# Kernel optimization log

Hardware: AMD Instinct MI355X
Metric: run time of the kernel (lower is better)

The kernel has to match this reference:

```python
import jax, jax.numpy as jnp
from jax import lax
import numpy as np

DIM, K, OUT_DIM = 128, 64, 256
SAMPLE_STEP = 30  # eval mode
WIN = 200


def _l2n(v, axis):
    return v / jnp.maximum(jnp.linalg.norm(v, axis=axis, keepdims=True), 1e-12)


def _conv(x, w, b, pad):
    y = lax.conv_general_dilated(x, w, (1, 1), [(pad, pad), (pad, pad)],
                                 dimension_numbers=('NCHW', 'OIHW', 'NCHW'))
    return y + b[None, :, None, None]


def _maxpool(x, kh, kw, sh, sw, ph, pw):
    return lax.reduce_window(x, -jnp.inf, lax.max, (1, 1, kh, kw), (1, 1, sh, sw),
                             [(0, 0), (0, 0), (ph, ph), (pw, pw)])


def setup_inputs() -> dict:
    key = jax.random.key(0)
    ks = jax.random.split(key, 12)
    s = 1.0 / np.sqrt(DIM)
    return {
        'x': jax.random.normal(ks[0], (4, DIM, 48, 900), jnp.float32),
        'cluster_centers': jax.random.uniform(ks[1], (K, DIM), jnp.float32) * s,
        'conv_w': jax.random.normal(ks[2], (K, DIM), jnp.float32) * s * 0.1,
        'conv_b': jax.random.normal(ks[3], (K,), jnp.float32) * s * 0.1,
        'w1': jax.random.normal(ks[4], (2 * DIM, DIM, 5, 5), jnp.float32) * 0.02,
        'b1': jnp.zeros((2 * DIM,), jnp.float32),
        'w2': jax.random.normal(ks[5], (4 * DIM, 2 * DIM, 5, 5), jnp.float32) * 0.01,
        'b2': jnp.zeros((4 * DIM,), jnp.float32),
        'w3': jax.random.normal(ks[6], (8 * DIM, 4 * DIM, 5, 5), jnp.float32) * 0.01,
        'b3': jnp.zeros((8 * DIM,), jnp.float32),
        'mlp_w': jax.random.normal(ks[7], (OUT_DIM, DIM * (K + 8)), jnp.float32) * s * 0.01,
        'mlp_b': jax.random.normal(ks[8], (OUT_DIM,), jnp.float32) * s * 0.01,
    }


def reference(x, cluster_centers, conv_w, conv_b, w1, b1, w2, b2, w3, b3, mlp_w, mlp_b):
    N, C, H, W = x.shape  # (4, 128, 48, 900)
    # ---- soft assignment (1x1 conv), softmax over clusters ----
    logits = jnp.einsum('nchw,kc->nkhw', x, conv_w) + conv_b[None, :, None, None]
    a = jax.nn.softmax(logits, axis=1)  # softmax over K (per spatial pos)
    # ---- residual-weighted sum over H, fused (avoids (N,K,C,HW) tensor) ----
    # sum_h a[n,k,h,w] * (x[n,c,h,w] - centers[k,c])
    xa = jnp.einsum('nkhw,nchw->nkcw', a, x)
    a_sum = a.sum(axis=2)  # (N,K,W)
    res = xa - cluster_centers[None, :, :, None] * a_sum[:, :, None, :]  # (N,K,C,W)
    # ---- x_conv feature branch on circularly padded input ----
    xp = jnp.concatenate([x[..., 800:], x, x[..., :100]], axis=-1)  # (N,C,H,1100)
    h = jax.nn.leaky_relu(_conv(xp, w1, b1, 2), 0.2)
    h = _maxpool(h, 3, 3, 3, 1, 0, 1)          # (N,256,16,1100)
    h = jax.nn.leaky_relu(_conv(h, w2, b2, 2), 0.2)
    h = _maxpool(h, 4, 5, 4, 1, 0, 2)          # (N,512,4,1100)
    h = _conv(h, w3, b3, 2)
    h = _maxpool(h, 4, WIN, 4, 1, 0, 0)        # (N,1024,1,901)
    xf = h[:, :, 0, ::SAMPLE_STEP][..., :-1]   # (N,1024,30)
    xf = _l2n(jnp.transpose(xf, (0, 2, 1)), axis=2)  # (N,30,1024)
    n_win = xf.shape[1]
    # ---- windowed VLAD pooling via cumsum (equiv to unfold(200, step).sum) ----
    resp = jnp.concatenate([res[..., 800:], res, res[..., :100]], axis=-1)  # (N,K,C,1100)
    cs = jnp.concatenate([jnp.zeros_like(resp[..., :1]), jnp.cumsum(resp, axis=-1)], axis=-1)
    starts = jnp.arange(n_win) * SAMPLE_STEP  # last window dropped, matching [:-1]
    vlad = cs[..., starts + WIN] - cs[..., starts]  # (N,K,C,30)
    vlad = jnp.transpose(vlad, (0, 3, 1, 2))        # (N,30,K,C)
    vlad = _l2n(vlad, axis=3)                        # intra-norm per cluster
    vlad = _l2n(vlad.reshape(N * n_win, K * C), axis=1)
    feat = jnp.concatenate([vlad, xf.reshape(N * n_win, -1)], axis=1)  # (N*30, 9216)
    out = _l2n(feat @ mlp_w.T + mlp_b, axis=1)
    return out.reshape(N, n_win, -1)
```

## Files before the change

### kernel.cpp

```cpp
#include <hip/hip_runtime.h>
#include <hip/hip_bf16.h>

#define NB   4
#define DIM  128
#define KC   64
#define HH   48
#define WW   900
#define WPAD 1100
#define WST  1160
#define NT   30
#define OC1  256
#define OC2  512
#define OC3  1024

typedef __attribute__((ext_vector_type(8))) short bf16x8;
typedef __attribute__((ext_vector_type(4))) float f32x4;
typedef unsigned short u16;
typedef unsigned int u32;

__device__ __forceinline__ u16 f2bf(float f){
  __hip_bfloat16 h = __float2bfloat16(f);
  u16 u; __builtin_memcpy(&u, &h, 2); return u;
}
__device__ __forceinline__ float bf2f(u16 u){
  __hip_bfloat16 h; __builtin_memcpy(&h, &u, 2); return __bfloat162float(h);
}

typedef __attribute__((address_space(1))) const u32 g_u32;
typedef __attribute__((address_space(3))) u32 l_u32;
__device__ __forceinline__ void gll16(const void* g, void* l){
  __builtin_amdgcn_global_load_lds((g_u32*)g, (l_u32*)l, 16, 0, 0);
}


__global__ __launch_bounds__(256) void vlad_softmax(const float* __restrict__ x,
    const float* __restrict__ conv_w, const float* __restrict__ conv_b, float* __restrict__ a){
  __shared__ float cwT[DIM*KC];
  __shared__ float cbs[KC];
  int t = threadIdx.x;
  for (int i = t; i < DIM*KC; i += 256){ int c = i >> 6, k = i & 63; cwT[i] = conv_w[k*DIM + c]; }
  if (t < KC) cbs[t] = conv_b[t];
  __syncthreads();
  int w = blockIdx.x*256 + t, h = blockIdx.y, n = blockIdx.z;
  bool ok = (w < WW);
  float lg[KC];
  #pragma unroll
  for (int k = 0; k < KC; ++k) lg[k] = cbs[k];
  const float* xp = x + (size_t)n*DIM*HH*WW + (size_t)h*WW + (ok ? w : 0);
  for (int c = 0; c < DIM; ++c){
    float xv = ok ? xp[(size_t)c*HH*WW] : 0.f;
    const float* cw = &cwT[c*KC];
    #pragma unroll
    for (int k = 0; k < KC; ++k) lg[k] += xv * cw[k];
  }
  float m = lg[0];
  #pragma unroll
  for (int k = 1; k < KC; ++k) m = fmaxf(m, lg[k]);
  float s = 0.f;
  #pragma unroll
  for (int k = 0; k < KC; ++k){ lg[k] = __expf(lg[k]-m); s += lg[k]; }
  float inv = 1.f/s;
  if (ok){
    float* dst = a + (((size_t)(n*HH + h))*WW + w)*KC;
    #pragma unroll
    for (int k = 0; k < KC; k += 4){
      float4 v = make_float4(lg[k]*inv, lg[k+1]*inv, lg[k+2]*inv, lg[k+3]*inv);
      *(float4*)&dst[k] = v;
    }
  }
}

__global__ __launch_bounds__(256) void vlad_xa3(const float* __restrict__ x, const float* __restrict__ a,
    const float* __restrict__ centers, float* __restrict__ ps){
  __shared__ float xw[2][10][132];
  __shared__ float aw[2][10][64];
  int t = threadIdx.x, s = blockIdx.x, n = blockIdx.y;
  int k = t >> 2, cb4 = t & 3;
  int p0 = s*10;
  int w0 = (p0 < 100) ? p0 + 800 : ((p0 < 1000) ? p0 - 100 : p0 - 1000);
  const float* xn = x + (size_t)n*DIM*HH*WW + w0;
  const float* an = a + (size_t)n*HH*WW*KC + (size_t)w0*KC;

  auto load = [&](int h, int buf){
    if (t < 128){
      const float* xr = xn + ((size_t)t*HH + h)*WW;
      #pragma unroll
      for (int w = 0; w < 10; ++w) xw[buf][w][t] = xr[w];
    } else {
      const float* ar = an + (size_t)h*WW*KC;
      int e0 = (t - 128)*5;
      #pragma unroll
      for (int q = 0; q < 5; ++q){ int e = e0 + q; aw[buf][e >> 6][e & 63] = ar[e]; }
    }
  };

  float acc[32];
  #pragma unroll
  for (int j = 0; j < 32; ++j) acc[j] = 0.f;
  float Sacc = 0.f;

  load(0, 0);
  for (int h = 0; h < HH; ++h){
    int buf = h & 1;
    __syncthreads();
    if (h + 1 < HH) load(h + 1, buf ^ 1);
    #pragma unroll 2
    for (int w = 0; w < 10; ++w){
      float av = aw[buf][w][k];
      Sacc += av;
      const float4* xr4 = (const float4*)&xw[buf][w][cb4*32];
      #pragma unroll
      for (int jj = 0; jj < 8; ++jj){
        float4 xv = xr4[jj];
        acc[jj*4+0] += av*xv.x; acc[jj*4+1] += av*xv.y;
        acc[jj*4+2] += av*xv.z; acc[jj*4+3] += av*xv.w;
      }
    }
    __syncthreads();
  }

  const float* ck = centers + (size_t)k*DIM + cb4*32;
  float* dst = ps + (((size_t)(n*KC + k))*110 + s)*DIM + cb4*32;
  #pragma unroll
  for (int jj = 0; jj < 8; ++jj){
    float4 o;
    o.x = acc[jj*4+0] - ck[jj*4+0]*Sacc;
    o.y = acc[jj*4+1] - ck[jj*4+1]*Sacc;
    o.z = acc[jj*4+2] - ck[jj*4+2]*Sacc;
    o.w = acc[jj*4+3] - ck[jj*4+3]*Sacc;
    *(float4*)&dst[jj*4] = o;
  }
}

__global__ __launch_bounds__(128) void vlad_win2(const float* __restrict__ ps, float* __restrict__ vlad){
  int c = threadIdx.x, k = blockIdx.x, tt = blockIdx.y, n = blockIdx.z;
  const float* base = ps + ((size_t)(n*KC + k))*110*DIM + c;
  float v = 0.f;
  #pragma unroll
  for (int u = 0; u < 20; ++u) v += base[(3*tt + u)*DIM];
  float ss = v*v;
  #pragma unroll
  for (int m = 1; m < 64; m <<= 1) ss += __shfl_xor(ss, m);
  __shared__ float red[2];
  if ((c & 63) == 0) red[c >> 6] = ss;
  __syncthreads();
  float tot = red[0] + red[1];
  float inv = 1.f / fmaxf(sqrtf(tot), 1e-12f);
  vlad[(((size_t)(n*NT + tt))*KC + k)*DIM + c] = v*inv;
}

__global__ __launch_bounds__(256) void vlad_gnorm(float* __restrict__ vlad){
  int row = blockIdx.x, t = threadIdx.x;
  float4* v = (float4*)(vlad + (size_t)row*(KC*DIM));
  float4 r[8]; float ss = 0.f;
  #pragma unroll
  for (int i = 0; i < 8; ++i){
    r[i] = v[t + i*256];
    ss += r[i].x*r[i].x + r[i].y*r[i].y + r[i].z*r[i].z + r[i].w*r[i].w;
  }
  #pragma unroll
  for (int m = 1; m < 64; m <<= 1) ss += __shfl_xor(ss, m);
  __shared__ float red[4];
  if ((t & 63) == 0) red[t >> 6] = ss;
  __syncthreads();
  float tot = red[0]+red[1]+red[2]+red[3];
  float inv = 1.f / fmaxf(sqrtf(tot), 1e-12f);
  #pragma unroll
  for (int i = 0; i < 8; ++i){
    float4 o = r[i]; o.x*=inv; o.y*=inv; o.z*=inv; o.w*=inv;
    v[t + i*256] = o;
  }
}


__global__ __launch_bounds__(256) void build_xpb(const float* __restrict__ x, u16* __restrict__ xpb){
  __shared__ u16 tile[DIM][33];
  int t = threadIdx.x, h = blockIdx.y, n = blockIdx.z;
  int b0 = blockIdx.x*32;
  #pragma unroll
  for (int i = 0; i < 16; ++i){
    int e = t + i*256;
    int c = e >> 5, bl = e & 31;
    int b = b0 + bl, w = b - 2;
    float v = 0.f;
    if (w >= 0 && w < WPAD){
      int wsrc = (w + 800) % 900;
      v = x[((size_t)(n*DIM + c)*HH + h)*WW + wsrc];
    }
    tile[c][bl] = f2bf(v);
  }
  __syncthreads();
  #pragma unroll
  for (int i = 0; i < 16; ++i){
    int e = t + i*256;
    int bl = e >> 7, c = e & 127;
    int b = b0 + bl;
    if (b < WST) xpb[((size_t)(n*HH + h)*WST + b)*DIM + c] = tile[c][bl];
  }
}

__global__ __launch_bounds__(256) void pack_w2(const float* __restrict__ w, u16* __restrict__ wp,
    int OC, int IC, int NICB){
  int idx = blockIdx.x*256 + threadIdx.x;
  int total = OC*IC*25;
  if (idx >= total) return;
  int e = idx & 7;
  int q = idx >> 3;
  int oc = q % OC;  int q2 = q / OC;
  int lgp = q2 & 3; int k0i = (q2 >> 2) & 3;
  int q3 = q2 >> 4;
  int icb = q3 % NICB; int tap = q3 / NICB;
  int ic = icb*128 + k0i*32 + lgp*8 + e;
  wp[idx] = f2bf(w[((size_t)oc*IC + ic)*25 + tap]);
}

template<int IC, int OC, int H>
__global__ __launch_bounds__(256,2) void conv5x5(const u16* __restrict__ in, const u16* __restrict__ wp,
    const float* __restrict__ bias, u16* __restrict__ out){
  constexpr int NICB = IC/128;
  constexpr int LN = (NICB==1?0:(NICB==2?1:2));
  __shared__ u16 sIn[2][132*128];
  int t = threadIdx.x;
  int wave = t >> 6, lane = t & 63, lr = lane & 15, lgp = lane >> 4;
  int w0  = blockIdx.x * 128;
  int ocb = blockIdx.y * 256;
  int nh = blockIdx.z; int n = nh / H, h = nh % H;
  int wo_oc = wave*64;
  f32x4 acc[4][8] = {};
  const u16* inN = in + (size_t)n*H*WST*IC;
  const size_t laneA = (size_t)(ocb + wo_oc + lr)*8;
  int dhlo = (2-h > 0) ? (2-h) : 0;
  int dhhi = (H+1-h < 4) ? (H+1-h) : 4;
  int nslab = (dhhi - dhlo + 1) << LN;

  auto stage = [&](int slab_, int buf_){
    int dh = dhlo + (slab_ >> LN);
    int icb = slab_ & (NICB-1);
    const u16* rowbase = inN + (size_t)(h + dh - 2)*WST*IC + (size_t)icb*128;
    for (int i = wave; i < 33; i += 4){
      int qq = i*64 + lane;
      int r = qq >> 4, cp = qq & 15;
      int c = cp ^ (r & 7);
      gll16(rowbase + (size_t)(w0 + r)*IC + c*8, &sIn[buf_][i*512]);
    }
  };

  stage(0, 0);
  __syncthreads();

  for (int slab = 0; slab < nslab; ++slab){
    int buf = slab & 1;
    if (slab + 1 < nslab) stage(slab + 1, buf ^ 1);
    int dh = dhlo + (slab >> LN);
    int icb = slab & (NICB-1);
    const u16* wslab = wp + (size_t)(dh*5*NICB + icb)*16*OC*8 + laneA;
    const u16* sB = &sIn[buf][0];
    bf16x8 Abuf[3][4];
    #pragma unroll
    for (int pi = 0; pi < 2; ++pi){
      const u16* ap = wslab + (size_t)((pi >> 2)*NICB*16 + ((pi & 3)*4 + lgp))*OC*8;
      #pragma unroll
      for (int ja = 0; ja < 4; ++ja) Abuf[pi][ja] = *(const bf16x8*)(ap + (size_t)ja*16*8);
    }
    #pragma unroll
    for (int dw = 0; dw < 5; ++dw){
      #pragma unroll
      for (int k0i = 0; k0i < 4; ++k0i){
        constexpr int NI = 20;
        const int i = dw*4 + k0i;
        {
          const int pn = (i + 2 < NI) ? (i + 2) : (NI - 1);
          const u16* ap = wslab + (size_t)((pn >> 2)*NICB*16 + ((pn & 3)*4 + lgp))*OC*8;
          #pragma unroll
          for (int ja = 0; ja < 4; ++ja) Abuf[(i + 2) % 3][ja] = *(const bf16x8*)(ap + (size_t)ja*16*8);
        }
        bf16x8 B[8];
        #pragma unroll
        for (int jb = 0; jb < 8; ++jb){
          int br = jb*16 + lr + dw;
          B[jb] = *(const bf16x8*)&sB[br*128 + (((k0i*4 + lgp) ^ (br & 7)) << 3)];
        }
        __builtin_amdgcn_s_setprio(1);
        #pragma unroll
        for (int ja = 0; ja < 4; ++ja)
          #pragma unroll
          for (int jb = 0; jb < 8; ++jb)
            acc[ja][jb] = __builtin_amdgcn_mfma_f32_16x16x32_bf16(Abuf[i % 3][ja], B[jb], acc[ja][jb], 0, 0, 0);
        __builtin_amdgcn_s_setprio(0);
      }
    }
    __syncthreads();
  }

  u16* outP = out + ((size_t)(n*H + h)*WST + 2)*OC;
  #pragma unroll
  for (int ja = 0; ja < 4; ++ja){
    int oc = ocb + wo_oc + ja*16 + lgp*4;
    float4 bv = *(const float4*)&bias[oc];
    #pragma unroll
    for (int jb = 0; jb < 8; ++jb){
      int wg = w0 + jb*16 + lr;
      if (wg < WPAD){
        f32x4 av = acc[ja][jb];
        ushort4 o;
        o.x = f2bf(av[0] + bv.x);
        o.y = f2bf(av[1] + bv.y);
        o.z = f2bf(av[2] + bv.z);
        o.w = f2bf(av[3] + bv.w);
        *(ushort4*)(outP + (size_t)wg*OC + oc) = o;
      }
    }
  }
}

__global__ __launch_bounds__(256) void pool1k(const u16* __restrict__ in, u16* __restrict__ out){
  int t = threadIdx.x;
  int wb = blockIdx.x*4 + (t >> 6);
  int oc = (t & 63)*4;
  int ho = blockIdx.y, n = blockIdx.z;
  int wo = wb - 2;
  float m0=0.f,m1=0.f,m2=0.f,m3=0.f;
  if (wo >= 0 && wo < WPAD){
    m0=m1=m2=m3=-1e30f;
    #pragma unroll
    for (int kh = 0; kh < 3; ++kh){
      const u16* row = in + ((size_t)(n*HH + ho*3 + kh)*WST + 2)*OC1 + oc;
      #pragma unroll
      for (int kw = 0; kw < 3; ++kw){
        int wi = wo - 1 + kw;
        if (wi >= 0 && wi < WPAD){
          ushort4 v = *(const ushort4*)(row + (size_t)wi*OC1);
          m0 = fmaxf(m0, bf2f(v.x)); m1 = fmaxf(m1, bf2f(v.y));
          m2 = fmaxf(m2, bf2f(v.z)); m3 = fmaxf(m3, bf2f(v.w));
        }
      }
    }
    m0 = (m0>0.f)?m0:0.2f*m0; m1 = (m1>0.f)?m1:0.2f*m1;
    m2 = (m2>0.f)?m2:0.2f*m2; m3 = (m3>0.f)?m3:0.2f*m3;
  }
  ushort4 o; o.x=f2bf(m0); o.y=f2bf(m1); o.z=f2bf(m2); o.w=f2bf(m3);
  *(ushort4*)(out + ((size_t)(n*16 + ho)*WST + wb)*OC1 + oc) = o;
}

__global__ __launch_bounds__(256) void pool2k(const u16* __restrict__ in, u16* __restrict__ out){
  int t = threadIdx.x;
  int wb = blockIdx.x*2 + (t >> 7);
  int oc = (t & 127)*4;
  int ho = blockIdx.y, n = blockIdx.z;
  int wo = wb - 2;
  float m0=0.f,m1=0.f,m2=0.f,m3=0.f;
  if (wo >= 0 && wo < WPAD){
    m0=m1=m2=m3=-1e30f;
    #pragma unroll
    for (int kh = 0; kh < 4; ++kh){
      const u16* row = in + ((size_t)(n*16 + ho*4 + kh)*WST + 2)*OC2 + oc;
      #pragma unroll
      for (int kw = 0; kw < 5; ++kw){
        int wi = wo - 2 + kw;
        if (wi >= 0 && wi < WPAD){
          ushort4 v = *(const ushort4*)(row + (size_t)wi*OC2);
          m0 = fmaxf(m0, bf2f(v.x)); m1 = fmaxf(m1, bf2f(v.y));
          m2 = fmaxf(m2, bf2f(v.z)); m3 = fmaxf(m3, bf2f(v.w));
        }
      }
    }
    m0 = (m0>0.f)?m0:0.2f*m0; m1 = (m1>0.f)?m1:0.2f*m1;
    m2 = (m2>0.f)?m2:0.2f*m2; m3 = (m3>0.f)?m3:0.2f*m3;
  }
  ushort4 o; o.x=f2bf(m0); o.y=f2bf(m1); o.z=f2bf(m2); o.w=f2bf(m3);
  *(ushort4*)(out + ((size_t)(n*4 + ho)*WST + wb)*OC2 + oc) = o;
}

__global__ __launch_bounds__(256) void pool3k(const u16* __restrict__ in, float* __restrict__ xfraw){
  int tt = blockIdx.x, hh = blockIdx.y, n = blockIdx.z;
  int oc = threadIdx.x*4;
  float m0=-1e30f,m1=-1e30f,m2=-1e30f,m3=-1e30f;
  const u16* row = in + ((size_t)(n*4 + hh)*WST + 2 + 30*tt)*OC3 + oc;
  for (int p = 0; p < 200; ++p){
    ushort4 v = *(const ushort4*)(row + (size_t)p*OC3);
    m0 = fmaxf(m0, bf2f(v.x)); m1 = fmaxf(m1, bf2f(v.y));
    m2 = fmaxf(m2, bf2f(v.z)); m3 = fmaxf(m3, bf2f(v.w));
  }
  float* dst = xfraw + (((size_t)(n*NT + tt))*4 + hh)*OC3 + oc;
  dst[0]=m0; dst[1]=m1; dst[2]=m2; dst[3]=m3;
}

__global__ __launch_bounds__(256) void xf_norm(const float* __restrict__ xfraw, float* __restrict__ xf){
  int row = blockIdx.x, t = threadIdx.x;
  const float* src = xfraw + (size_t)row*4096;
  float v[4]; float ss = 0.f;
  #pragma unroll
  for (int j = 0; j < 4; ++j){
    float m = src[t + j*256];
    #pragma unroll
    for (int hh = 1; hh < 4; ++hh) m = fmaxf(m, src[hh*1024 + t + j*256]);
    v[j] = m; ss += m*m;
  }
  #pragma unroll
  for (int m = 1; m < 64; m <<= 1) ss += __shfl_xor(ss, m);
  __shared__ float red[4];
  if ((t & 63) == 0) red[t >> 6] = ss;
  __syncthreads();
  float tot = red[0]+red[1]+red[2]+red[3];
  float inv = 1.f/fmaxf(sqrtf(tot), 1e-12f);
  float* dst = xf + (size_t)row*OC3;
  #pragma unroll
  for (int j = 0; j < 4; ++j) dst[t + j*256] = v[j]*inv;
}

__global__ __launch_bounds__(256) void mlp_part(const float* __restrict__ vlad, const float* __restrict__ xf,
    const float* __restrict__ W, float* __restrict__ part){
  __shared__ float feat[4][256];
  int kc = blockIdx.x, rb = blockIdx.y, t = threadIdx.x;
  int i0 = kc*256;
  #pragma unroll
  for (int r = 0; r < 4; ++r){
    int row = rb*4 + r;
    int i = i0 + t;
    feat[r][t] = (i < 8192) ? vlad[(size_t)row*8192 + i] : xf[(size_t)row*1024 + (i - 8192)];
  }
  __syncthreads();
  const float* wr = W + (size_t)t*9216 + i0;
  float a0=0.f, a1=0.f, a2=0.f, a3=0.f;
  for (int i = 0; i < 256; i += 4){
    float4 wv = *(const float4*)&wr[i];
    a0 += feat[0][i]*wv.x + feat[0][i+1]*wv.y + feat[0][i+2]*wv.z + feat[0][i+3]*wv.w;
    a1 += feat[1][i]*wv.x + feat[1][i+1]*wv.y + feat[1][i+2]*wv.z + feat[1][i+3]*wv.w;
    a2 += feat[2][i]*wv.x + feat[2][i+1]*wv.y + feat[2][i+2]*wv.z + feat[2][i+3]*wv.w;
    a3 += feat[3][i]*wv.x + feat[3][i+1]*wv.y + feat[3][i+2]*wv.z + feat[3][i+3]*wv.w;
  }
  float* p0 = part + (((size_t)(rb*4 + 0)*36 + kc))*256 + t;
  p0[0]          = a0;
  p0[36*256]     = a1;
  p0[2*36*256]   = a2;
  p0[3*36*256]   = a3;
}

__global__ __launch_bounds__(256) void mlp_reduce(const float* __restrict__ part, const float* __restrict__ b,
    float* __restrict__ out){
  int row = blockIdx.x, t = threadIdx.x;
  const float* pr = part + (size_t)row*36*256 + t;
  float acc = b[t];
  #pragma unroll
  for (int kc = 0; kc < 36; ++kc) acc += pr[kc*256];
  float ss = acc*acc;
  #pragma unroll
  for (int m = 1; m < 64; m <<= 1) ss += __shfl_xor(ss, m);
  __shared__ float red[4];
  if ((t & 63) == 0) red[t >> 6] = ss;
  __syncthreads();
  float tot = red[0]+red[1]+red[2]+red[3];
  float inv = 1.f/fmaxf(sqrtf(tot), 1e-12f);
  out[(size_t)row*256 + t] = acc*inv;
}

extern "C" void kernel_launch(void* const* d_in, const int* in_sizes, int n_in,
                              void* d_out, int out_size, void* d_ws, size_t ws_size,
                              hipStream_t stream){
  const float* x       = (const float*)d_in[0];
  const float* centers = (const float*)d_in[1];
  const float* conv_w  = (const float*)d_in[2];
  const float* conv_b  = (const float*)d_in[3];
  const float* w1      = (const float*)d_in[4];
  const float* b1      = (const float*)d_in[5];
  const float* w2      = (const float*)d_in[6];
  const float* b2      = (const float*)d_in[7];
  const float* w3      = (const float*)d_in[8];
  const float* b3      = (const float*)d_in[9];
  const float* mlp_w   = (const float*)d_in[10];
  const float* mlp_b   = (const float*)d_in[11];
  float* out = (float*)d_out;
  char* ws = (char*)d_ws;
  const size_t MB = 1ull << 20;
  if (ws_size < 248*MB) return;

  float* vlad  = (float*)(ws + 0);
  float* xf    = (float*)(ws + 4*MB);
  float* xfraw = (float*)(ws + 5*MB);
  char*  AR    = ws + 7*MB;
  float* a  = (float*)(AR + 85*MB);
  float* ps = (float*)(AR + 128*MB);
  u16* xpb = (u16*)(AR + 0);
  u16* wp1 = (u16*)(AR + 55*MB);
  u16* wp2 = (u16*)(AR + 57*MB);
  u16* wp3 = (u16*)(AR + 64*MB);
  u16* h1  = (u16*)(AR + 89*MB);
  u16* p1  = (u16*)(AR + 0);
  u16* h2  = (u16*)(AR + 89*MB);
  u16* p2  = (u16*)(AR + 163*MB);
  u16* h3  = (u16*)(AR + 0);
  float* part = (float*)(AR + 200*MB);

  vlad_softmax<<<dim3(4,HH,NB), 256, 0, stream>>>(x, conv_w, conv_b, a);
  vlad_xa3<<<dim3(110,NB), 256, 0, stream>>>(x, a, centers, ps);
  vlad_win2<<<dim3(KC,NT,NB), 128, 0, stream>>>(ps, vlad);
  vlad_gnorm<<<dim3(NB*NT), 256, 0, stream>>>(vlad);

  pack_w2<<<dim3(3200),  256, 0, stream>>>(w1, wp1, OC1, DIM, 1);
  pack_w2<<<dim3(12800), 256, 0, stream>>>(w2, wp2, OC2, OC1, 2);
  pack_w2<<<dim3(51200), 256, 0, stream>>>(w3, wp3, OC3, OC2, 4);
  build_xpb<<<dim3(37,HH,NB), 256, 0, stream>>>(x, xpb);
  conv5x5<128,256,48><<<dim3(9, OC1/256, NB*HH), 256, 0, stream>>>(xpb, wp1, b1, h1);
  pool1k<<<dim3(WST/4,16,NB), 256, 0, stream>>>(h1, p1);
  conv5x5<256,512,16><<<dim3(9, OC2/256, NB*16), 256, 0, stream>>>(p1, wp2, b2, h2);
  pool2k<<<dim3(WST/2,4,NB), 256, 0, stream>>>(h2, p2);
  conv5x5<512,1024,4><<<dim3(9, OC3/256, NB*4), 256, 0, stream>>>(p2, wp3, b3, h3);
  pool3k<<<dim3(NT,4,NB), 256, 0, stream>>>(h3, xfraw);
  xf_norm<<<dim3(NB*NT), 256, 0, stream>>>(xfraw, xf);

  mlp_part<<<dim3(36,30), 256, 0, stream>>>(vlad, xf, mlp_w, part);
  mlp_reduce<<<dim3(NB*NT), 256, 0, stream>>>(part, mlp_b, out);
}
```

Baseline: 1.574 ms.

## Remap conv blocks per XCD, deepen weight prefetch, split final pool into segments

The conv kernel now uses a flattened 1D grid. Blocks are remapped so that blocks on the same XCD (bid&7) share the same output-channel tile, which should improve L2 reuse of the packed weights. The weight register prefetch ring grows from depth 3 to 5 and now carries across slab boundaries, hiding global-load latency between slabs at the cost of more VGPRs. The final 200-wide max-pool is restructured into 10-column segment maxima reduced over H, then combined 20 at a time in xf_norm, which avoids re-reading overlapping windows.

```diff
diff --git a/kernel.cpp b/kernel.cpp
--- a/kernel.cpp
+++ b/kernel.cpp
@@ -219,12 +219,18 @@
     const float* __restrict__ bias, u16* __restrict__ out){
   constexpr int NICB = IC/128;
   constexpr int LN = (NICB==1?0:(NICB==2?1:2));
+  constexpr int Y = OC/256;
+  constexpr int XG = 8/Y;
   __shared__ u16 sIn[2][132*128];
   int t = threadIdx.x;
   int wave = t >> 6, lane = t & 63, lr = lane & 15, lgp = lane >> 4;
-  int w0  = blockIdx.x * 128;
-  int ocb = blockIdx.y * 256;
-  int nh = blockIdx.z; int n = nh / H, h = nh % H;
+  int bid = blockIdx.x;
+  int xcd = bid & 7, slot = bid >> 3;
+  int li = (xcd % XG) + XG*slot;
+  int w0  = (li % 9) * 128;
+  int nh  = li / 9;
+  int ocb = (xcd / XG) * 256;
+  int n = nh / H, h = nh % H;
   int wo_oc = wave*64;
   f32x4 acc[4][8] = {};
   const u16* inN = in + (size_t)n*H*WST*IC;
@@ -244,35 +250,44 @@
       gll16(rowbase + (size_t)(w0 + r)*IC + c*8, &sIn[buf_][i*512]);
     }
   };
+  auto wbase = [&](int slab_) -> const u16* {
+    int dh = dhlo + (slab_ >> LN);
+    int icb = slab_ & (NICB-1);
+    return wp + (size_t)(dh*5*NICB + icb)*16*OC*8 + laneA;
+  };
 
   stage(0, 0);
   __syncthreads();
+
+  bf16x8 Abuf[5][4];
+  {
+    const u16* w0p = wbase(0);
+    #pragma unroll
+    for (int pi = 0; pi < 4; ++pi){
+      const u16* ap = w0p + (size_t)((pi >> 2)*NICB*16 + ((pi & 3)*4 + lgp))*OC*8;
+      #pragma unroll
+      for (int ja = 0; ja < 4; ++ja) Abuf[pi][ja] = *(const bf16x8*)(ap + (size_t)ja*16*8);
+    }
+  }
 
   for (int slab = 0; slab < nslab; ++slab){
     int buf = slab & 1;
     if (slab + 1 < nslab) stage(slab + 1, buf ^ 1);
-    int dh = dhlo + (slab >> LN);
-    int icb = slab & (NICB-1);
-    const u16* wslab = wp + (size_t)(dh*5*NICB + icb)*16*OC*8 + laneA;
+    const u16* wslab  = wbase(slab);
+    const u16* wslabN = (slab + 1 < nslab) ? wbase(slab + 1) : wslab;
     const u16* sB = &sIn[buf][0];
-    bf16x8 Abuf[3][4];
-    #pragma unroll
-    for (int pi = 0; pi < 2; ++pi){
-      const u16* ap = wslab + (size_t)((pi >> 2)*NICB*16 + ((pi & 3)*4 + lgp))*OC*8;
-      #pragma unroll
-      for (int ja = 0; ja < 4; ++ja) Abuf[pi][ja] = *(const bf16x8*)(ap + (size_t)ja*16*8);
-    }
     #pragma unroll
     for (int dw = 0; dw < 5; ++dw){
       #pragma unroll
       for (int k0i = 0; k0i < 4; ++k0i){
-        constexpr int NI = 20;
         const int i = dw*4 + k0i;
         {
-          const int pn = (i + 2 < NI) ? (i + 2) : (NI - 1);
-          const u16* ap = wslab + (size_t)((pn >> 2)*NICB*16 + ((pn & 3)*4 + lgp))*OC*8;
+          const int pn = i + 4;
+          const int pj = (pn < 20) ? pn : pn - 20;
+          const u16* psrc = (pn < 20) ? wslab : wslabN;
+          const u16* ap = psrc + (size_t)((pj >> 2)*NICB*16 + ((pj & 3)*4 + lgp))*OC*8;
           #pragma unroll
-          for (int ja = 0; ja < 4; ++ja) Abuf[(i + 2) % 3][ja] = *(const bf16x8*)(ap + (size_t)ja*16*8);
+          for (int ja = 0; ja < 4; ++ja) Abuf[pn % 5][ja] = *(const bf16x8*)(ap + (size_t)ja*16*8);
         }
         bf16x8 B[8];
         #pragma unroll
@@ -285,7 +300,7 @@
         for (int ja = 0; ja < 4; ++ja)
           #pragma unroll
           for (int jb = 0; jb < 8; ++jb)
-            acc[ja][jb] = __builtin_amdgcn_mfma_f32_16x16x32_bf16(Abuf[i % 3][ja], B[jb], acc[ja][jb], 0, 0, 0);
+            acc[ja][jb] = __builtin_amdgcn_mfma_f32_16x16x32_bf16(Abuf[i % 5][ja], B[jb], acc[ja][jb], 0, 0, 0);
         __builtin_amdgcn_s_setprio(0);
       }
     }
@@ -371,29 +386,35 @@
   *(ushort4*)(out + ((size_t)(n*4 + ho)*WST + wb)*OC2 + oc) = o;
 }
 
-__global__ __launch_bounds__(256) void pool3k(const u16* __restrict__ in, float* __restrict__ xfraw){
-  int tt = blockIdx.x, hh = blockIdx.y, n = blockIdx.z;
+__global__ __launch_bounds__(256) void pool3a(const u16* __restrict__ in, float* __restrict__ segmax){
+  int seg = blockIdx.x, n = blockIdx.y;
   int oc = threadIdx.x*4;
   float m0=-1e30f,m1=-1e30f,m2=-1e30f,m3=-1e30f;
-  const u16* row = in + ((size_t)(n*4 + hh)*WST + 2 + 30*tt)*OC3 + oc;
-  for (int p = 0; p < 200; ++p){
-    ushort4 v = *(const ushort4*)(row + (size_t)p*OC3);
-    m0 = fmaxf(m0, bf2f(v.x)); m1 = fmaxf(m1, bf2f(v.y));
-    m2 = fmaxf(m2, bf2f(v.z)); m3 = fmaxf(m3, bf2f(v.w));
-  }
-  float* dst = xfraw + (((size_t)(n*NT + tt))*4 + hh)*OC3 + oc;
+  #pragma unroll
+  for (int hh = 0; hh < 4; ++hh){
+    const u16* row = in + ((size_t)(n*4 + hh)*WST + 2 + seg*10)*OC3 + oc;
+    #pragma unroll
+    for (int p = 0; p < 10; ++p){
+      ushort4 v = *(const ushort4*)(row + (size_t)p*OC3);
+      m0 = fmaxf(m0, bf2f(v.x)); m1 = fmaxf(m1, bf2f(v.y));
+      m2 = fmaxf(m2, bf2f(v.z)); m3 = fmaxf(m3, bf2f(v.w));
+    }
+  }
+  float* dst = segmax + ((size_t)n*110 + seg)*1024 + oc;
   dst[0]=m0; dst[1]=m1; dst[2]=m2; dst[3]=m3;
 }
 
-__global__ __launch_bounds__(256) void xf_norm(const float* __restrict__ xfraw, float* __restrict__ xf){
+__global__ __launch_bounds__(256) void xf_norm(const float* __restrict__ segmax, float* __restrict__ xf){
   int row = blockIdx.x, t = threadIdx.x;
-  const float* src = xfraw + (size_t)row*4096;
+  int n = row / NT, tt = row % NT;
+  const float* base = segmax + (size_t)n*110*1024;
   float v[4]; float ss = 0.f;
   #pragma unroll
   for (int j = 0; j < 4; ++j){
-    float m = src[t + j*256];
-    #pragma unroll
-    for (int hh = 1; hh < 4; ++hh) m = fmaxf(m, src[hh*1024 + t + j*256]);
+    int oc = t + j*256;
+    float m = -1e30f;
+    #pragma unroll
+    for (int u = 0; u < 20; ++u) m = fmaxf(m, base[(size_t)(3*tt + u)*1024 + oc]);
     v[j] = m; ss += m*m;
   }
   #pragma unroll
@@ -500,12 +521,12 @@
   pack_w2<<<dim3(12800), 256, 0, stream>>>(w2, wp2, OC2, OC1, 2);
   pack_w2<<<dim3(51200), 256, 0, stream>>>(w3, wp3, OC3, OC2, 4);
   build_xpb<<<dim3(37,HH,NB), 256, 0, stream>>>(x, xpb);
-  conv5x5<128,256,48><<<dim3(9, OC1/256, NB*HH), 256, 0, stream>>>(xpb, wp1, b1, h1);
+  conv5x5<128,256,48><<<dim3(9*1*(NB*48)), 256, 0, stream>>>(xpb, wp1, b1, h1);
   pool1k<<<dim3(WST/4,16,NB), 256, 0, stream>>>(h1, p1);
-  conv5x5<256,512,16><<<dim3(9, OC2/256, NB*16), 256, 0, stream>>>(p1, wp2, b2, h2);
+  conv5x5<256,512,16><<<dim3(9*2*(NB*16)), 256, 0, stream>>>(p1, wp2, b2, h2);
   pool2k<<<dim3(WST/2,4,NB), 256, 0, stream>>>(h2, p2);
-  conv5x5<512,1024,4><<<dim3(9, OC3/256, NB*4), 256, 0, stream>>>(p2, wp3, b3, h3);
-  pool3k<<<dim3(NT,4,NB), 256, 0, stream>>>(h3, xfraw);
+  conv5x5<512,1024,4><<<dim3(9*4*(NB*4)), 256, 0, stream>>>(p2, wp3, b3, h3);
+  pool3a<<<dim3(110,NB), 256, 0, stream>>>(h3, xfraw);
   xf_norm<<<dim3(NB*NT), 256, 0, stream>>>(xfraw, xf);
 
   mlp_part<<<dim3(36,30), 256, 0, stream>>>(vlad, xf, mlp_w, part);
```

After: 1.737 ms. 10.4% more time.
